# Kernel tuning notes

Measured on AMD Instinct MI355X. Metric: run time of the kernel, lower is better.

Reference implementation:

```python
import jax, jax.numpy as jnp
import numpy as np

A0 = 0.529177249
SIGMA = jnp.array([0.5515909, 1.8886297, 1.3225029, 1.2316629, 2.1884933, 1.7750372, 1.3677907, 1.3820058], dtype=jnp.float32)
N_MOL, N_ATOM, N_SPECIES = 512, 64, 4
AEV_LEN, RADIAL_LEN = 384, 32
DIN = AEV_LEN + RADIAL_LEN + 2  # 418
DIMS = (256, 192, 160)
ETA, RC = 4.0, 10.0  # stand-in radial-qaev constants (Bohr)
RS = jnp.linspace(0.8, 9.0, RADIAL_LEN, dtype=jnp.float32)


def _celu(x):
    return jax.nn.celu(x, alpha=0.1)


def _mlp(x, W0, b0, W1, b1, W2, b2, W3, b3):
    h = _celu(x @ W0 + b0)
    h = _celu(h @ W1 + b1)
    h = _celu(h @ W2 + b2)
    return (h @ W3 + b3)[:, 0]


def _dispatch(x, species_flat, W0, b0, W1, b1, W2, b2, W3, b3):
    # per-species expert MLP routing; padded atoms (species==-1) stay 0
    out = jnp.zeros(x.shape[0], x.dtype)
    for s in range(N_SPECIES):
        ys = _mlp(x, W0[s], b0[s], W1[s], b1[s], W2[s], b2[s], W3[s], b3[s])
        out = jnp.where(species_flat == s, ys, out)
    return out


def _radial_qaev(d, charges, pair_nodiag):
    # stand-in for compute_radial_qaev: charge-weighted radial symmetry functions
    fc = jnp.where(d < RC, 0.5 * jnp.cos(np.pi * d / RC) + 0.5, 0.0)
    g = 0.25 * jnp.exp(-ETA * (d[..., None] - RS) ** 2) * (fc * pair_nodiag)[..., None]  # [N,n,n,R]
    return jnp.einsum('nijr,nj->nir', g, charges)


def _esperf(pair_mask, diag_mask, d, charges, sig):
    s = jnp.maximum(sig[:, None, :] ** 2 + sig[:, :, None] ** 2, 1e-8)
    j_ij = jax.scipy.special.erf(d / jnp.sqrt(2.0 * s)) / d
    return (charges[:, :, None] * j_ij * pair_mask * diag_mask[None]).sum(axis=-2)


def _forward(species, coordinates, net_charge, aev, chi_params, ani_params):
    N, n = species.shape
    diff = coordinates[:, None, :, :] - coordinates[:, :, None, :]
    d = jnp.sqrt((diff * diff).sum(-1) + 1e-16) / A0  # Bohr, [N,n,n]
    sig = SIGMA[species]  # species==-1 wraps to last entry, matching torch
    inv_jii = np.sqrt(np.pi).astype(np.float32) * sig  # 1 / (1/sqrt(pi)/sig)
    pm = (species != -1).astype(d.dtype)
    pair_mask = pm[:, None, :] * pm[:, :, None]
    diag_mask = 1.0 - jnp.eye(n, dtype=d.dtype)
    pair_nodiag = pair_mask * diag_mask
    species_flat = species.reshape(-1)
    aevf = aev.reshape(N * n, -1)
    q = jnp.zeros((N, n), d.dtype)
    esp = jnp.zeros((N, n), d.dtype)
    qraev = _radial_qaev(d, q, pair_nodiag)
    for _ in range(2):  # charge equilibration loop
        feats = jnp.concatenate([aevf, qraev.reshape(N * n, -1), q.reshape(-1, 1), esp.reshape(-1, 1)], axis=1)
        chi = _dispatch(feats, species_flat, *chi_params).reshape(N, n)
        corr = (net_charge + (chi * inv_jii).sum(1)) / (inv_jii * pm).sum(1)
        q = -inv_jii * (chi - corr[:, None]) * pm
        esp = _esperf(pair_mask, diag_mask, d, q, sig)
        qraev = _radial_qaev(d, q, pair_nodiag)
    feats = jnp.concatenate([aevf, qraev.reshape(N * n, -1), q.reshape(-1, 1), esp.reshape(-1, 1)], axis=1)
    ae = _dispatch(feats, species_flat, *ani_params).reshape(N, n)
    charge_sq = q[:, None, :] * q[:, :, None] * pair_mask
    coulomb = charge_sq * jax.nn.sigmoid((d - 2.2) * 8.5) / d  # elect_screen
    elec = jnp.triu(coulomb, k=1).sum(axis=(1, 2))
    return ae.sum(1) + elec, q


def setup_inputs() -> dict:
    key = jax.random.key(0)
    ks = jax.random.split(key, 5)
    species = jax.random.randint(ks[0], (N_MOL, N_ATOM), -1, N_SPECIES)  # -1 = padding
    coordinates = jax.random.uniform(ks[1], (N_MOL, N_ATOM, 3), jnp.float32) * 10.0
    net_charge = jnp.zeros((N_MOL,), jnp.float32)
    aev = jax.random.normal(ks[2], (N_MOL, N_ATOM, AEV_LEN), jnp.float32)
    inp = {'species': species, 'coordinates': coordinates, 'net_charge': net_charge, 'aev': aev}
    dims = (DIN,) + DIMS + (1,)
    for name, k in (('chi', ks[3]), ('ani', ks[4])):
        lks = jax.random.split(k, 4)
        for i in range(4):
            inp[f'{name}_W{i}'] = jax.random.normal(lks[i], (N_SPECIES, dims[i], dims[i + 1]), jnp.float32) / float(np.sqrt(dims[i]))
            inp[f'{name}_b{i}'] = jnp.zeros((N_SPECIES, dims[i + 1]), jnp.float32)
    return inp


def reference(species, coordinates, net_charge, aev,
              chi_W0, chi_b0, chi_W1, chi_b1, chi_W2, chi_b2, chi_W3, chi_b3,
              ani_W0, ani_b0, ani_W1, ani_b1, ani_W2, ani_b2, ani_W3, ani_b3):
    chi_params = (chi_W0, chi_b0, chi_W1, chi_b1, chi_W2, chi_b2, chi_W3, chi_b3)
    ani_params = (ani_W0, ani_b0, ani_W1, ani_b1, ani_W2, ani_b2, ani_W3, ani_b3)
    energy, q = _forward(species, coordinates, net_charge, aev, chi_params, ani_params)
    return (species, energy, q)
```

## Files before the change

### kernel.cpp

```cpp
#include <hip/hip_runtime.h>
#include <math.h>

#define NMOL 512
#define NATOM 64
#define NFLAT (NMOL*NATOM)
#define AEVL 384
#define FK 448
#define D0 256
#define D1 192
#define D2 160
#define MPAD 33024

typedef _Float16 h8 __attribute__((ext_vector_type(8)));
typedef float    f4 __attribute__((ext_vector_type(4)));

__constant__ float c_sigma[8] = {0.5515909f,1.8886297f,1.3225029f,1.2316629f,
                                 2.1884933f,1.7750372f,1.3677907f,1.3820058f};

__device__ __forceinline__ float wsum(float v){
  #pragma unroll
  for (int o=1;o<64;o<<=1) v += __shfl_xor(v,o);
  return v;
}

__device__ __forceinline__ void gll16(const _Float16* g, _Float16* l){
  __builtin_amdgcn_global_load_lds(
    (const __attribute__((address_space(1))) void*)g,
    (__attribute__((address_space(3))) void*)l, 16, 0, 0);
}

__global__ void wtrans_all(const float* __restrict__ W0c, const float* __restrict__ W1c,
                           const float* __restrict__ W2c, const float* __restrict__ W0a,
                           const float* __restrict__ W1a, const float* __restrict__ W2a,
                           _Float16* __restrict__ T0c, _Float16* __restrict__ T1c,
                           _Float16* __restrict__ T2c, _Float16* __restrict__ T0a,
                           _Float16* __restrict__ T1a, _Float16* __restrict__ T2a){
  int u = blockIdx.x*256 + threadIdx.x;
  int s = blockIdx.y;
  int ani = blockIdx.z;
  const float* W; _Float16* T; int K, N, KT;
  if (u < 14336){            W = ani?W0a:W0c; T = ani?T0a:T0c; K=418; N=256; KT=14; }
  else if (u < 20480){ u -= 14336; W = ani?W1a:W1c; T = ani?T1a:T1c; K=256; N=192; KT=8; }
  else               { u -= 20480; W = ani?W2a:W2c; T = ani?T2a:T2c; K=192; N=160; KT=6; }
  int col = u % N;
  int pk  = u / N;
  int part = pk & 3, kt = pk >> 2;
  h8 o;
  #pragma unroll
  for (int e=0;e<8;e++){
    int gk = kt*32 + part*8 + e;
    float v = (gk < K) ? W[((size_t)s*K + gk)*N + col] : 0.f;
    o[e] = (_Float16)v;
  }
  *reinterpret_cast<h8*>(T + ((size_t)s*KT*4 + pk)*N*8 + (size_t)col*8) = o;
}

__global__ void prep_kernel(const int* __restrict__ species,
                            const float* __restrict__ coord,
                            const float* __restrict__ aev,
                            float* __restrict__ dbuf, float* __restrict__ sig,
                            float* __restrict__ invj, float* __restrict__ pmf,
                            int* __restrict__ blkhist, _Float16* __restrict__ feat){
  int m = blockIdx.x, t = threadIdx.x;
  __shared__ float c[192];
  if (t < 192) c[t] = coord[m*192 + t];
  __syncthreads();
  #pragma unroll
  for (int k=0;k<16;k++){
    int p = t + 256*k;
    int i = p >> 6, j = p & 63;
    float dx=c[i*3]-c[j*3], dy=c[i*3+1]-c[j*3+1], dz=c[i*3+2]-c[j*3+2];
    dbuf[m*4096 + p] = sqrtf(dx*dx+dy*dy+dz*dz + 1e-16f) / 0.529177249f;
  }
  if (t < 64){
    int g = m*64+t;
    int s = species[g];
    float sg = c_sigma[s < 0 ? 7 : s];
    sig[g]  = sg;
    invj[g] = 1.7724539f * sg;
    pmf[g]  = (s>=0) ? 1.f : 0.f;
    #pragma unroll
    for (int sp=0;sp<4;sp++){
      unsigned long long mask = __ballot(s==sp);
      if (t==0) blkhist[m*4+sp] = __popcll(mask);
    }
  }
  const float* aevm = aev + (size_t)m*64*AEVL;
  _Float16* featm = feat + (size_t)m*64*FK;
  for (int j=t; j<64*56; j+=256){
    int al = j/56, cc = j - (j/56)*56;
    int k8 = cc*8;
    h8 o;
    if (k8 < AEVL){
      const f4* sp = reinterpret_cast<const f4*>(aevm + (size_t)al*AEVL + k8);
      f4 a = sp[0], b = sp[1];
      o[0]=(_Float16)a[0]; o[1]=(_Float16)a[1]; o[2]=(_Float16)a[2]; o[3]=(_Float16)a[3];
      o[4]=(_Float16)b[0]; o[5]=(_Float16)b[1]; o[6]=(_Float16)b[2]; o[7]=(_Float16)b[3];
    } else {
      #pragma unroll
      for (int e=0;e<8;e++) o[e] = (_Float16)0.f;
    }
    *reinterpret_cast<h8*>(featm + (size_t)al*FK + k8) = o;
  }
}

__global__ void plan_kernel(const int* __restrict__ blkhist, int* __restrict__ meta,
                            int* __restrict__ blkoff){
  __shared__ int h[NMOL*4];
  __shared__ int tot[4], base[4];
  int t = threadIdx.x;
  for (int j=t; j<NMOL*4; j+=256) h[j] = blkhist[j];
  __syncthreads();
  if (t < 4){
    int sum = 0;
    for (int m=0;m<NMOL;m++) sum += h[m*4+t];
    tot[t] = sum;
  }
  __syncthreads();
  if (t == 0){
    int b=0, tb=0;
    meta[4]=0; meta[9]=0;
    for (int s=0;s<4;s++){
      meta[s] = tot[s];
      base[s] = b;
      int tiles = (tot[s]+63)>>6;
      b  += tiles<<6;  tb += tiles;
      meta[5+s]  = b;  meta[10+s] = tb;
    }
  }
  __syncthreads();
  if (t < 4){
    int run = base[t];
    for (int m=0;m<NMOL;m++){ int v = h[m*4+t]; h[m*4+t] = run; run += v; }
  }
  __syncthreads();
  for (int j=t; j<NMOL*4; j+=256) blkoff[j] = h[j];
}

__global__ void scatter_kernel(const int* __restrict__ species,
                               const int* __restrict__ blkoff,
                               int* __restrict__ idxarr){
  int m = blockIdx.x, a = threadIdx.x, g = m*64+a;
  int s = species[g];
  unsigned long long below = (1ull<<a) - 1ull;
  #pragma unroll
  for (int sp=0;sp<4;sp++){
    unsigned long long mask = __ballot(s==sp);
    if (s==sp){
      int rank = __popcll(mask & below);
      idxarr[blkoff[m*4+sp] + rank] = g;
    }
  }
}

template<int GATHER, int NCB, int KTW, int FUSEL3>
__launch_bounds__(256)
__global__ void gemm_gll(const _Float16* __restrict__ Ah,
                         const _Float16* __restrict__ feat,
                         const int* __restrict__ idxarr,
                         const int* __restrict__ meta,
                         const _Float16* __restrict__ Wt,
                         const float* __restrict__ Ball,
                         _Float16* __restrict__ C,
                         const float* __restrict__ W3a,
                         const float* __restrict__ b3a,
                         float* __restrict__ outv,
                         int N, int ktrun, int act){
  constexpr int COLS = NCB*16;
  constexpr int NB16 = COLS/16;
  int t = blockIdx.x;
  if (t >= meta[13]) return;
  int s = 0;
  while (s < 3 && t >= meta[10+s]) s++;
  int trow = t - meta[9+s];
  int row0 = meta[4+s] + (trow<<6);
  int mrem = meta[s] - (trow<<6); if (mrem > 64) mrem = 64;
  int c0 = blockIdx.y * COLS;

  __shared__ __align__(16) _Float16 Ab[2][2048];
  __shared__ __align__(16) _Float16 Bb[2][COLS*32];

  int tid = threadIdx.x;
  int w = tid>>6, l = tid&63, lr16 = l&15, lg = l>>4;

  int arow = row0 + l;
  int amax = row0 + mrem - 1;
  if (arow > amax) arow = amax;
  const _Float16* asrc;
  if (GATHER) asrc = feat + (size_t)idxarr[arow]*FK;
  else        asrc = Ah + (size_t)arow*(KTW*32);

  const _Float16* Wbase = Wt + (size_t)s*KTW*4*N*8 + (size_t)c0*8;

  auto STAGE = [&](int buf, int kt){
    gll16(asrc + kt*32 + w*8, &Ab[buf][w*512]);
    for (int j=w; j<NB16; j+=4){
      int u = j*64 + l;
      int part = u / COLS, col = u - part*COLS;
      gll16(Wbase + ((size_t)(kt*4+part)*N + col)*8, &Bb[buf][j*512]);
    }
  };

  f4 acc[NCB];
  #pragma unroll
  for (int c=0;c<NCB;c++){ acc[c][0]=0.f; acc[c][1]=0.f; acc[c][2]=0.f; acc[c][3]=0.f; }

  STAGE(0, 0);
  __syncthreads();
  int cur = 0;
  for (int kt=0; kt<ktrun; ++kt){
    if (kt+1 < ktrun) STAGE(cur^1, kt+1);
    h8 aF = *reinterpret_cast<const h8*>(&Ab[cur][lg*512 + (w*16+lr16)*8]);
    #pragma unroll
    for (int c=0;c<NCB;c++){
      h8 bF = *reinterpret_cast<const h8*>(&Bb[cur][lg*COLS*8 + (c*16+lr16)*8]);
      acc[c] = __builtin_amdgcn_mfma_f32_16x16x32_f16(aF, bF, acc[c], 0, 0, 0);
    }
    if (kt+1 < ktrun){
      __syncthreads();
      cur ^= 1;
    }
  }

  const float* bias = Ball + s*N;
  if (FUSEL3){
    const float* w3 = W3a + s*COLS;
    float vrow[4] = {0.f,0.f,0.f,0.f};
    #pragma unroll
    for (int c=0;c<NCB;c++){
      int col = c*16 + lr16;
      float bsv = bias[col];
      float wv  = w3[col];
      #pragma unroll
      for (int rr=0;rr<4;rr++){
        float vv = acc[c][rr] + bsv;
        vv = vv > 0.f ? vv : 0.1f*expm1f(vv*10.f);
        vrow[rr] += vv * wv;
      }
    }
    float b3v = b3a[s];
    #pragma unroll
    for (int rr=0;rr<4;rr++){
      float v = vrow[rr];
      #pragma unroll
      for (int o=1;o<16;o<<=1) v += __shfl_xor(v, o);
      int lrow = w*16 + lg*4 + rr;
      if (lr16 == 0 && lrow < mrem)
        outv[idxarr[row0+lrow]] = v + b3v;
    }
  } else {
    #pragma unroll
    for (int c=0;c<NCB;c++){
      int col = c0 + c*16 + lr16;
      float bsv = bias[col];
      #pragma unroll
      for (int rr=0;rr<4;rr++){
        int lrow = w*16 + lg*4 + rr;
        if (lrow >= mrem) continue;
        float vv = acc[c][rr] + bsv;
        if (act) vv = vv > 0.f ? vv : 0.1f*expm1f(vv*10.f);
        C[(size_t)(row0+lrow)*N + col] = (_Float16)vv;
      }
    }
  }
}

__global__ void iter_kernel(const float* __restrict__ chi, const float* __restrict__ invj,
                            const float* __restrict__ pmf, const float* __restrict__ netq,
                            const float* __restrict__ dbuf, const float* __restrict__ sig,
                            float* __restrict__ q, _Float16* __restrict__ feat){
  int m = blockIdx.x, tid = threadIdx.x;
  int i = tid & 63, w = tid >> 6;
  __shared__ float qs[64], pms[64], sg2[64];
  __shared__ float esp8[8][64];
  __shared__ float qr[8][64][8];
  if (tid < 64){
    int g = m*64 + i;
    float pm = pmf[g], ij = invj[g];
    float c = pm > 0.f ? chi[g] : 0.f;
    float num = wsum(c*ij);
    float den = wsum(ij*pm);
    float corr = (netq[m] + num) / den;
    float qa = -ij*(c - corr)*pm;
    q[g] = qa;
    feat[(size_t)g*FK + 416] = (_Float16)qa;
    qs[i] = qa; pms[i] = pm;
    float s0 = sig[g]; sg2[i] = s0*s0;
  }
  __syncthreads();
  const float* dr = dbuf + (size_t)m*4096;
  {
    float si2 = sg2[i];
    float acc = 0.f;
    #pragma unroll
    for (int jj=0;jj<8;jj++){
      int j = w*8 + jj;
      if (j==i) continue;
      float d = dr[j*64 + i];
      float ss = fmaxf(si2 + sg2[j], 1e-8f);
      acc += qs[j]*pms[j]*erff(d/sqrtf(2.f*ss))/d;
    }
    esp8[w][i] = acc;
  }
  {
    const float STEP = 0.264516129f;
    const float C2 = 0.7558781f;
    const float C1 = 0.5713518f;
    int jh = w>>2, bg = w&3;
    float rbase = 0.8f + (bg*8)*STEP;
    float pmi = pms[i];
    float acc[8] = {0.f,0.f,0.f,0.f,0.f,0.f,0.f,0.f};
    for (int jj=0;jj<32;jj++){
      int j = jh*32 + jj;
      if (j==i) continue;
      float d = dr[j*64+i];
      if (d < 10.f){
        float wq = 0.25f*(0.5f*__cosf(0.31415927f*d)+0.5f)*qs[j]*pms[j]*pmi;
        if (wq != 0.f){
          float t0 = d - rbase;
          float fv = __expf(-4.f*t0*t0);
          float gv = __expf(2.116129f*t0)*C2;
          #pragma unroll
          for (int r=0;r<8;r++){ acc[r] += wq*fv; fv *= gv; gv *= C1; }
        }
      }
    }
    #pragma unroll
    for (int r=0;r<8;r++) qr[w][i][r] = acc[r];
  }
  __syncthreads();
  if (tid < 64){
    int g = m*64+i;
    float e = 0.f;
    #pragma unroll
    for (int k=0;k<8;k++) e += esp8[k][i];
    feat[(size_t)g*FK + 417] = (_Float16)(e * pms[i]);
  }
  if (tid < 256){
    int ii = tid & 63, bg = tid >> 6;
    h8 o;
    #pragma unroll
    for (int r=0;r<8;r++) o[r] = (_Float16)(qr[bg][ii][r] + qr[bg+4][ii][r]);
    *reinterpret_cast<h8*>(feat + (size_t)(m*64+ii)*FK + 384 + bg*8) = o;
  }
}

__global__ void final_kernel(const float* __restrict__ dbuf, const float* __restrict__ q,
                             const float* __restrict__ pmf, const float* __restrict__ ae,
                             const int* __restrict__ species, float* __restrict__ out){
  int m = blockIdx.x, a = threadIdx.x, g = m*64+a;
  __shared__ float qs[64], pms[64];
  qs[a]=q[g]; pms[a]=pmf[g];
  __syncthreads();
  float acc=0.f;
  const float* dr = dbuf + (size_t)m*4096;
  for (int b=0;b<64;b++){
    if (b==a) continue;
    float d = dr[b*64+a];
    float sgm = 1.f/(1.f+__expf(-(d-2.2f)*8.5f));
    acc += qs[b]*pms[b]*sgm/d;
  }
  float e = 0.5f*qs[a]*pms[a]*acc;
  float aea = pms[a]>0.f ? ae[g] : 0.f;
  float tot = wsum(e + aea);
  if (a == 0) out[NFLAT + m] = tot;
  out[g] = (float)species[g];
  out[NFLAT + NMOL + g] = qs[a];
}

extern "C" void kernel_launch(void* const* d_in, const int* in_sizes, int n_in,
                              void* d_out, int out_size, void* d_ws, size_t ws_size,
                              hipStream_t stream){
  const int*   species = (const int*)d_in[0];
  const float* coord   = (const float*)d_in[1];
  const float* netq    = (const float*)d_in[2];
  const float* aev     = (const float*)d_in[3];
  const float* cW[4] = {(const float*)d_in[4],(const float*)d_in[6],(const float*)d_in[8],(const float*)d_in[10]};
  const float* cB[4] = {(const float*)d_in[5],(const float*)d_in[7],(const float*)d_in[9],(const float*)d_in[11]};
  const float* aW[4] = {(const float*)d_in[12],(const float*)d_in[14],(const float*)d_in[16],(const float*)d_in[18]};
  const float* aB[4] = {(const float*)d_in[13],(const float*)d_in[15],(const float*)d_in[17],(const float*)d_in[19]};

  float* f = (float*)d_ws;
  size_t o = 0;
  float* dbuf  = f + o; o += (size_t)NMOL*4096;
  float* sig   = f + o; o += NFLAT;
  float* invj  = f + o; o += NFLAT;
  float* pmf   = f + o; o += NFLAT;
  float* q     = f + o; o += NFLAT;
  float* chi   = f + o; o += NFLAT;
  _Float16* feat = (_Float16*)(f + o); o += (size_t)NFLAT*FK/2;
  _Float16* h0h  = (_Float16*)(f + o); o += (size_t)MPAD*D0/2;
  _Float16* h1h  = (_Float16*)(f + o); o += (size_t)MPAD*D1/2;
  const int KT_[3] = {14, 8, 6};
  const int N_[3]  = {D0, D1, D2};
  _Float16* wt[6];
  for (int i=0;i<6;i++){
    wt[i] = (_Float16*)(f + o);
    o += (size_t)4*KT_[i%3]*N_[i%3]*32/2;
  }
  int* meta    = (int*)(f + o); o += 64;
  int* idxarr  = (int*)(f + o); o += MPAD;
  int* blkhist = (int*)(f + o); o += NMOL*4;
  int* blkoff  = (int*)(f + o); o += NMOL*4;

  prep_kernel<<<dim3(NMOL), 256, 0, stream>>>(species, coord, aev, dbuf, sig, invj, pmf,
                                              blkhist, feat);
  wtrans_all<<<dim3(95, 4, 2), 256, 0, stream>>>(cW[0], cW[1], cW[2], aW[0], aW[1], aW[2],
                                                 wt[0], wt[1], wt[2], wt[3], wt[4], wt[5]);
  plan_kernel<<<dim3(1), 256, 0, stream>>>(blkhist, meta, blkoff);
  scatter_kernel<<<dim3(NMOL), 64, 0, stream>>>(species, blkoff, idxarr);

  for (int pass=0; pass<3; ++pass){
    int wb = (pass<2) ? 0 : 3;
    const float* const* Bp = (pass<2) ? cB : aB;
    const float* W3 = (pass<2) ? cW[3] : aW[3];
    const float* b3 = (pass<2) ? cB[3] : aB[3];
    int kt0 = (pass==0) ? 12 : 14;
    gemm_gll<1,8,14,0><<<dim3(516,2), 256, 0, stream>>>(nullptr, feat, idxarr, meta,
                                                        wt[wb+0], Bp[0], h0h,
                                                        nullptr, nullptr, nullptr, D0, kt0, 1);
    gemm_gll<0,6,8,0><<<dim3(516,2), 256, 0, stream>>>(h0h, nullptr, idxarr, meta,
                                                       wt[wb+1], Bp[1], h1h,
                                                       nullptr, nullptr, nullptr, D1, 8, 1);
    gemm_gll<0,10,6,1><<<dim3(516,1), 256, 0, stream>>>(h1h, nullptr, idxarr, meta,
                                                        wt[wb+2], Bp[2], nullptr,
                                                        W3, b3, chi, D2, 6, 1);
    if (pass < 2)
      iter_kernel<<<dim3(NMOL), 512, 0, stream>>>(chi, invj, pmf, netq, dbuf, sig, q, feat);
  }
  final_kernel<<<dim3(NMOL), 64, 0, stream>>>(dbuf, q, pmf, chi, species, (float*)d_out);
}
```

Measured before the change: 263.6 us.

## Precompute AEV-part of first layer once for all passes, add only charge-dependent K tiles

The first-layer GEMM's contribution from the static AEV columns (first 12 K-tiles) is computed once for both chi and ani weights in a dual-accumulator pass and stored as fp16 partial sums. Later passes only multiply the remaining 2 K-tiles that depend on updated charges and add the stored partial. This removes repeated GEMM work over the large AEV input. The cost is extra fp16 buffer traffic for the partials and some added rounding from storing the partial sums in fp16.

```diff
diff --git a/kernel.cpp b/kernel.cpp
--- a/kernel.cpp
+++ b/kernel.cpp
@@ -153,21 +153,25 @@
   }
 }
 
-template<int GATHER, int NCB, int KTW, int FUSEL3>
+template<int GATHER, int NCB, int KTW, int MODE>
 __launch_bounds__(256)
 __global__ void gemm_gll(const _Float16* __restrict__ Ah,
                          const _Float16* __restrict__ feat,
                          const int* __restrict__ idxarr,
                          const int* __restrict__ meta,
                          const _Float16* __restrict__ Wt,
+                         const _Float16* __restrict__ Wt2,
                          const float* __restrict__ Ball,
                          _Float16* __restrict__ C,
                          const float* __restrict__ W3a,
                          const float* __restrict__ b3a,
                          float* __restrict__ outv,
-                         int N, int ktrun, int act){
+                         _Float16* __restrict__ P1,
+                         _Float16* __restrict__ P2,
+                         int N, int ktoff, int ktrun, int act){
   constexpr int COLS = NCB*16;
   constexpr int NB16 = COLS/16;
+  constexpr int BPAN = (MODE==2) ? 2 : 1;
   int t = blockIdx.x;
   if (t >= meta[13]) return;
   int s = 0;
@@ -178,7 +182,7 @@
   int c0 = blockIdx.y * COLS;
 
   __shared__ __align__(16) _Float16 Ab[2][2048];
-  __shared__ __align__(16) _Float16 Bb[2][COLS*32];
+  __shared__ __align__(16) _Float16 Bb[2][BPAN*COLS*32];
 
   int tid = threadIdx.x;
   int w = tid>>6, l = tid&63, lr16 = l&15, lg = l>>4;
@@ -187,10 +191,11 @@
   int amax = row0 + mrem - 1;
   if (arow > amax) arow = amax;
   const _Float16* asrc;
-  if (GATHER) asrc = feat + (size_t)idxarr[arow]*FK;
-  else        asrc = Ah + (size_t)arow*(KTW*32);
-
-  const _Float16* Wbase = Wt + (size_t)s*KTW*4*N*8 + (size_t)c0*8;
+  if (GATHER) asrc = feat + (size_t)idxarr[arow]*FK + ktoff*32;
+  else        asrc = Ah + (size_t)arow*(KTW*32) + ktoff*32;
+
+  const _Float16* Wbase  = Wt  + ((size_t)s*KTW*4 + (size_t)ktoff*4)*N*8 + (size_t)c0*8;
+  const _Float16* Wbase2 = (MODE==2) ? (Wt2 + ((size_t)s*KTW*4)*N*8 + (size_t)c0*8) : nullptr;
 
   auto STAGE = [&](int buf, int kt){
     gll16(asrc + kt*32 + w*8, &Ab[buf][w*512]);
@@ -198,12 +203,19 @@
       int u = j*64 + l;
       int part = u / COLS, col = u - part*COLS;
       gll16(Wbase + ((size_t)(kt*4+part)*N + col)*8, &Bb[buf][j*512]);
+      if (MODE==2)
+        gll16(Wbase2 + ((size_t)(kt*4+part)*N + col)*8, &Bb[buf][COLS*32 + j*512]);
     }
   };
 
   f4 acc[NCB];
+  f4 acc2[(MODE==2)?NCB:1];
   #pragma unroll
   for (int c=0;c<NCB;c++){ acc[c][0]=0.f; acc[c][1]=0.f; acc[c][2]=0.f; acc[c][3]=0.f; }
+  if (MODE==2){
+    #pragma unroll
+    for (int c=0;c<NCB;c++){ acc2[c][0]=0.f; acc2[c][1]=0.f; acc2[c][2]=0.f; acc2[c][3]=0.f; }
+  }
 
   STAGE(0, 0);
   __syncthreads();
@@ -216,6 +228,13 @@
       h8 bF = *reinterpret_cast<const h8*>(&Bb[cur][lg*COLS*8 + (c*16+lr16)*8]);
       acc[c] = __builtin_amdgcn_mfma_f32_16x16x32_f16(aF, bF, acc[c], 0, 0, 0);
     }
+    if (MODE==2){
+      #pragma unroll
+      for (int c=0;c<NCB;c++){
+        h8 bF = *reinterpret_cast<const h8*>(&Bb[cur][COLS*32 + lg*COLS*8 + (c*16+lr16)*8]);
+        acc2[c] = __builtin_amdgcn_mfma_f32_16x16x32_f16(aF, bF, acc2[c], 0, 0, 0);
+      }
+    }
     if (kt+1 < ktrun){
       __syncthreads();
       cur ^= 1;
@@ -223,7 +242,7 @@
   }
 
   const float* bias = Ball + s*N;
-  if (FUSEL3){
+  if (MODE==1){
     const float* w3 = W3a + s*COLS;
     float vrow[4] = {0.f,0.f,0.f,0.f};
     #pragma unroll
@@ -247,6 +266,39 @@
       int lrow = w*16 + lg*4 + rr;
       if (lr16 == 0 && lrow < mrem)
         outv[idxarr[row0+lrow]] = v + b3v;
+    }
+  } else if (MODE==2){
+    #pragma unroll
+    for (int c=0;c<NCB;c++){
+      int col = c0 + c*16 + lr16;
+      float bsv = bias[col];
+      #pragma unroll
+      for (int rr=0;rr<4;rr++){
+        int lrow = w*16 + lg*4 + rr;
+        if (lrow >= mrem) continue;
+        size_t idx = (size_t)(row0+lrow)*N + col;
+        float p1 = acc[c][rr], p2 = acc2[c][rr];
+        P1[idx] = (_Float16)p1;
+        P2[idx] = (_Float16)p2;
+        float vv = p1 + bsv;
+        vv = vv > 0.f ? vv : 0.1f*expm1f(vv*10.f);
+        C[idx] = (_Float16)vv;
+      }
+    }
+  } else if (MODE==3){
+    #pragma unroll
+    for (int c=0;c<NCB;c++){
+      int col = c0 + c*16 + lr16;
+      float bsv = bias[col];
+      #pragma unroll
+      for (int rr=0;rr<4;rr++){
+        int lrow = w*16 + lg*4 + rr;
+        if (lrow >= mrem) continue;
+        size_t idx = (size_t)(row0+lrow)*N + col;
+        float vv = acc[c][rr] + (float)P1[idx] + bsv;
+        vv = vv > 0.f ? vv : 0.1f*expm1f(vv*10.f);
+        C[idx] = (_Float16)vv;
+      }
     }
   } else {
     #pragma unroll
@@ -391,6 +443,8 @@
   _Float16* feat = (_Float16*)(f + o); o += (size_t)NFLAT*FK/2;
   _Float16* h0h  = (_Float16*)(f + o); o += (size_t)MPAD*D0/2;
   _Float16* h1h  = (_Float16*)(f + o); o += (size_t)MPAD*D1/2;
+  _Float16* h0preC = (_Float16*)(f + o); o += (size_t)MPAD*D0/2;
+  _Float16* h0preA = (_Float16*)(f + o); o += (size_t)MPAD*D0/2;
   const int KT_[3] = {14, 8, 6};
   const int N_[3]  = {D0, D1, D2};
   _Float16* wt[6];
@@ -410,21 +464,31 @@
   plan_kernel<<<dim3(1), 256, 0, stream>>>(blkhist, meta, blkoff);
   scatter_kernel<<<dim3(NMOL), 64, 0, stream>>>(species, blkoff, idxarr);
 
+  gemm_gll<1,8,14,2><<<dim3(516,2), 256, 0, stream>>>(nullptr, feat, idxarr, meta,
+                                                      wt[0], wt[3], cB[0], h0h,
+                                                      nullptr, nullptr, nullptr,
+                                                      h0preC, h0preA, D0, 0, 12, 1);
+
   for (int pass=0; pass<3; ++pass){
     int wb = (pass<2) ? 0 : 3;
     const float* const* Bp = (pass<2) ? cB : aB;
     const float* W3 = (pass<2) ? cW[3] : aW[3];
     const float* b3 = (pass<2) ? cB[3] : aB[3];
-    int kt0 = (pass==0) ? 12 : 14;
-    gemm_gll<1,8,14,0><<<dim3(516,2), 256, 0, stream>>>(nullptr, feat, idxarr, meta,
-                                                        wt[wb+0], Bp[0], h0h,
-                                                        nullptr, nullptr, nullptr, D0, kt0, 1);
+    if (pass > 0){
+      _Float16* pre = (pass==1) ? h0preC : h0preA;
+      gemm_gll<1,8,14,3><<<dim3(516,2), 256, 0, stream>>>(nullptr, feat, idxarr, meta,
+                                                          wt[wb+0], nullptr, Bp[0], h0h,
+                                                          nullptr, nullptr, nullptr,
+                                                          pre, nullptr, D0, 12, 2, 1);
+    }
     gemm_gll<0,6,8,0><<<dim3(516,2), 256, 0, stream>>>(h0h, nullptr, idxarr, meta,
-                                                       wt[wb+1], Bp[1], h1h,
-                                                       nullptr, nullptr, nullptr, D1, 8, 1);
+                                                       wt[wb+1], nullptr, Bp[1], h1h,
+                                                       nullptr, nullptr, nullptr,
+                                                       nullptr, nullptr, D1, 0, 8, 1);
     gemm_gll<0,10,6,1><<<dim3(516,1), 256, 0, stream>>>(h1h, nullptr, idxarr, meta,
-                                                        wt[wb+2], Bp[2], nullptr,
-                                                        W3, b3, chi, D2, 6, 1);
+                                                        wt[wb+2], nullptr, Bp[2], nullptr,
+                                                        W3, b3, chi,
+                                                        nullptr, nullptr, D2, 0, 6, 1);
     if (pass < 2)
       iter_kernel<<<dim3(NMOL), 512, 0, stream>>>(chi, invj, pmf, netq, dbuf, sig, q, feat);
   }
```

Result: no change. 268.4 us (+1.8%).
